# Performance work log

Hardware: AMD Instinct MI355X
Metric: run time of the kernel (lower is better)

Reference implementation:

```python
import jax, jax.numpy as jnp
import numpy as np

B, S, D = 2, 2048, 1024
H = 16
HD = D // H

def setup_inputs() -> dict:
    key = jax.random.key(0)
    ks = jax.random.split(key, 6)
    sc = 0.02
    return {
        'x': jax.random.normal(ks[0], (B, S, D), jnp.float32),
        'Wq': jax.random.normal(ks[1], (D, D), jnp.float32) * sc,
        'Wk': jax.random.normal(ks[2], (D, D), jnp.float32) * sc,
        'Wv': jax.random.normal(ks[3], (D, D), jnp.float32) * sc,
        'Wo': jax.random.normal(ks[4], (D, D), jnp.float32) * sc,
        'bo': jnp.zeros((D,), jnp.float32),
    }

def reference(x, Wq, Wk, Wv, Wo, bo):
    b, s, d_in = x.shape
    # torch Linear: y = x @ W.T
    q = jnp.einsum('bsd,ed->bse', x, Wq)
    k = jnp.einsum('bsd,ed->bse', x, Wk)
    v = jnp.einsum('bsd,ed->bse', x, Wv)
    # [b, h, s, hd]
    q = q.reshape(b, s, H, HD).transpose(0, 2, 1, 3)
    k = k.reshape(b, s, H, HD).transpose(0, 2, 1, 3)
    v = v.reshape(b, s, H, HD).transpose(0, 2, 1, 3)
    # NOTE: original divides by sqrt(d_out), not sqrt(head_dim)
    scores = jnp.einsum('bhqd,bhkd->bhqk', q, k) / jnp.sqrt(jnp.float32(D))
    causal = jnp.tril(jnp.ones((s, s), dtype=bool))  # True = keep
    scores = jnp.where(causal[None, None], scores, -jnp.inf)
    attn = jax.nn.softmax(scores, axis=-1)
    ctx = jnp.einsum('bhqk,bhkd->bhqd', attn, v)
    ctx = ctx.transpose(0, 2, 1, 3).reshape(b, s, D)
    return jnp.einsum('bsd,ed->bse', ctx, Wo) + bo
```

## Files before the change

kernel.cpp:

```cpp
#include <hip/hip_runtime.h>
#include <hip/hip_bf16.h>
#include <stdint.h>

typedef unsigned short u16;
typedef __attribute__((ext_vector_type(8))) short short8;
typedef __attribute__((ext_vector_type(4))) float f32x4;
typedef __attribute__((ext_vector_type(16))) float f32x16;
typedef __attribute__((ext_vector_type(4))) u16 u16x4;

#define NB 2
#define NS 2048
#define ND 1024
#define NH 16
#define NM 4096

#define QSCALE 0.045084220f

#if __has_builtin(__builtin_amdgcn_exp2f)
#define EXP2(x) __builtin_amdgcn_exp2f(x)
#else
__device__ __forceinline__ float __exp2_asm(float x){
  float r;
  asm("v_exp_f32 %0, %1" : "=v"(r) : "v"(x));
  return r;
}
#define EXP2(x) __exp2_asm(x)
#endif
#if __has_builtin(__builtin_amdgcn_rcpf)
#define RCP(x) __builtin_amdgcn_rcpf(x)
#else
#define RCP(x) (1.0f / (x))
#endif

__device__ __forceinline__ u16 f2bf(float f){
  union { float f; unsigned u; } v; v.f = f;
  unsigned r = v.u + 0x7fff + ((v.u >> 16) & 1);
  return (u16)(r >> 16);
}

__device__ __forceinline__ unsigned cvtpk(float lo, float hi){
  unsigned r;
  asm("v_cvt_pk_bf16_f32 %0, %1, %2" : "=v"(r) : "v"(lo), "v"(hi));
  return r;
}

__device__ __forceinline__ void pl32swap(unsigned &e, unsigned &o){
  asm("v_permlane32_swap_b32 %0, %1" : "+v"(e), "+v"(o));
}

__device__ __forceinline__ void gload_lds16(const u16* g, u16* l){
  __builtin_amdgcn_global_load_lds(
      (const __attribute__((address_space(1))) unsigned int*)g,
      (__attribute__((address_space(3))) unsigned int*)l, 16, 0, 0);
}

__device__ __forceinline__ f32x16 mfma32(short8 a, short8 b, f32x16 c){
  return __builtin_amdgcn_mfma_f32_32x32x16_bf16(a, b, c, 0, 0, 0);
}

__global__ void cvt_kernel(const float* __restrict__ src, u16* __restrict__ dst, int n){
  int i = (blockIdx.x * blockDim.x + threadIdx.x) * 4;
  if (i < n){
    float4 v = *(const float4*)(src + i);
    u16x4 o = { f2bf(v.x), f2bf(v.y), f2bf(v.z), f2bf(v.w) };
    *(u16x4*)(dst + i) = o;
  }
}

__global__ void cvt4_kernel(const float* __restrict__ a, const float* __restrict__ b,
                            const float* __restrict__ c, const float* __restrict__ d,
                            u16* __restrict__ oa, u16* __restrict__ ob,
                            u16* __restrict__ oc, u16* __restrict__ od){
  const float* s; u16* o;
  switch (blockIdx.y){
    case 0: s = a; o = oa; break;
    case 1: s = b; o = ob; break;
    case 2: s = c; o = oc; break;
    default: s = d; o = od; break;
  }
  int i = (blockIdx.x * blockDim.x + threadIdx.x) * 4;
  float4 v = *(const float4*)(s + i);
  u16x4 pk = { f2bf(v.x), f2bf(v.y), f2bf(v.z), f2bf(v.w) };
  *(u16x4*)(o + i) = pk;
}

__device__ __forceinline__ void gemm_core(
    const u16* __restrict__ A, const u16* __restrict__ W,
    int m0, int n0, u16* lsA, u16* lsB, f32x4 acc[4][4])
{
  const int tid = threadIdx.x;
  const int l   = tid & 63;
  const int wr  = (tid >> 7) & 1;
  const int wc  = (tid >> 6) & 1;
  const int lr  = l & 15;
  const int lkb = (l >> 4) << 4;
  const int sr  = tid >> 3;
  const int scb = (tid & 7) << 4;

  for (int kt = 0; kt < 16; ++kt){
    const int k0 = kt << 6;
    #pragma unroll
    for (int i = 0; i < 4; ++i){
      int r   = (i << 5) + sr;
      int cbs = scb ^ ((r & 7) << 4);
      gload_lds16(&A[(size_t)(m0 + r) * ND + k0 + (cbs >> 1)], &lsA[r * 64 + (scb >> 1)]);
      gload_lds16(&W[(size_t)(n0 + r) * ND + k0 + (cbs >> 1)], &lsB[r * 64 + (scb >> 1)]);
    }
    __syncthreads();

    short8 af[4][2], bf[4][2];
    #pragma unroll
    for (int m16 = 0; m16 < 4; ++m16){
      int r  = (wr << 6) + (m16 << 4) + lr;
      int rx = (r & 7) << 4;
      #pragma unroll
      for (int ks = 0; ks < 2; ++ks){
        int off = r * 128 + (((ks << 6) + lkb) ^ rx);
        af[m16][ks] = *(const short8*)((const char*)lsA + off);
      }
    }
    #pragma unroll
    for (int n16 = 0; n16 < 4; ++n16){
      int r  = (wc << 6) + (n16 << 4) + lr;
      int rx = (r & 7) << 4;
      #pragma unroll
      for (int ks = 0; ks < 2; ++ks){
        int off = r * 128 + (((ks << 6) + lkb) ^ rx);
        bf[n16][ks] = *(const short8*)((const char*)lsB + off);
      }
    }
    #pragma unroll
    for (int m16 = 0; m16 < 4; ++m16)
      #pragma unroll
      for (int n16 = 0; n16 < 4; ++n16){
        acc[m16][n16] = __builtin_amdgcn_mfma_f32_16x16x32_bf16(af[m16][0], bf[n16][0], acc[m16][n16], 0, 0, 0);
        acc[m16][n16] = __builtin_amdgcn_mfma_f32_16x16x32_bf16(af[m16][1], bf[n16][1], acc[m16][n16], 0, 0, 0);
      }
    __syncthreads();
  }
}

__global__ __launch_bounds__(256) void gemm_qkv(
    const u16* __restrict__ xb,
    const u16* __restrict__ Wqb, const u16* __restrict__ Wkb, const u16* __restrict__ Wvb,
    u16* __restrict__ Qo, u16* __restrict__ Ko, u16* __restrict__ Vt)
{
  __shared__ u16 lsA[128*64];
  __shared__ u16 lsB[128*64];
  const int z = blockIdx.z;
  const u16* W = (z == 0) ? Wqb : (z == 1) ? Wkb : Wvb;
  const int m0 = blockIdx.x << 7, n0 = blockIdx.y << 7;
  f32x4 acc[4][4] = {};
  gemm_core(xb, W, m0, n0, lsA, lsB, acc);

  const int l  = threadIdx.x & 63;
  const int wr = (threadIdx.x >> 7) & 1, wc = (threadIdx.x >> 6) & 1;
  const int rb = m0 + (wr << 6) + ((l >> 4) << 2);
  const int cb = n0 + (wc << 6) + (l & 15);

  if (z < 2){
    const float sc = (z == 0) ? QSCALE : 1.0f;
    u16* C = (z == 0) ? Qo : Ko;
    #pragma unroll
    for (int m16 = 0; m16 < 4; ++m16)
      #pragma unroll
      for (int n16 = 0; n16 < 4; ++n16)
        #pragma unroll
        for (int r = 0; r < 4; ++r)
          C[(size_t)(rb + (m16 << 4) + r) * ND + cb + (n16 << 4)] = f2bf(acc[m16][n16][r] * sc);
  } else {
    #pragma unroll
    for (int m16 = 0; m16 < 4; ++m16){
      int srow = rb + (m16 << 4);
      int bi = srow >> 11, s = srow & 2047;
      #pragma unroll
      for (int n16 = 0; n16 < 4; ++n16){
        int col = cb + (n16 << 4);
        u16x4 pk = { f2bf(acc[m16][n16][0]), f2bf(acc[m16][n16][1]),
                     f2bf(acc[m16][n16][2]), f2bf(acc[m16][n16][3]) };
        *(u16x4*)&Vt[((size_t)(bi * 16 + (col >> 6)) * 64 + (col & 63)) * 2048 + s] = pk;
      }
    }
  }
}

__global__ __launch_bounds__(256) void gemm_out(
    const u16* __restrict__ ctxb, const u16* __restrict__ Wob,
    const float* __restrict__ bo, float* __restrict__ out)
{
  __shared__ u16 lsA[128*64];
  __shared__ u16 lsB[128*64];
  const int m0 = blockIdx.x << 7, n0 = blockIdx.y << 7;
  f32x4 acc[4][4] = {};
  gemm_core(ctxb, Wob, m0, n0, lsA, lsB, acc);

  const int l  = threadIdx.x & 63;
  const int wr = (threadIdx.x >> 7) & 1, wc = (threadIdx.x >> 6) & 1;
  const int rb = m0 + (wr << 6) + ((l >> 4) << 2);
  const int cb = n0 + (wc << 6) + (l & 15);
  #pragma unroll
  for (int m16 = 0; m16 < 4; ++m16)
    #pragma unroll
    for (int n16 = 0; n16 < 4; ++n16)
      #pragma unroll
      for (int r = 0; r < 4; ++r){
        int col = cb + (n16 << 4);
        out[(size_t)(rb + (m16 << 4) + r) * ND + col] = acc[m16][n16][r] + bo[col];
      }
}

__device__ __forceinline__ void stage_tile(const u16* src, int srcStride, u16* lds, int tid){
  const int rl = tid >> 3;
  const int ch = tid & 7;
  const int cs = ch ^ (rl & 7);
  gload_lds16(&src[(size_t)rl * srcStride + cs * 8],        &lds[rl * 64 + ch * 8]);
  gload_lds16(&src[(size_t)(rl + 32) * srcStride + cs * 8], &lds[(rl + 32) * 64 + ch * 8]);
}

__device__ __forceinline__ void qk_tile(const u16* lsKt, const short8 qf[4],
                                        int q5, int hi, f32x16 &s0, f32x16 &s1){
  const char* Kc = (const char*)lsKt;
  const int swz = q5 & 7;
  f32x16 a = {}, b = {};
  __builtin_amdgcn_s_setprio(1);
  #pragma unroll
  for (int ks = 0; ks < 4; ++ks){
    int c0 = ((2 * ks + hi) ^ swz) << 4;
    short8 k0 = *(const short8*)(Kc + q5 * 128 + c0);
    short8 k1 = *(const short8*)(Kc + (q5 + 32) * 128 + c0);
    a = mfma32(k0, qf[ks], a);
    b = mfma32(k1, qf[ks], b);
  }
  __builtin_amdgcn_s_setprio(0);
  s0 = a; s1 = b;
}

__device__ __forceinline__ void sm_pv(f32x16 s0, f32x16 s1, const u16* lsVt,
                                      int t, int qb, int qgl, int q5, int hi,
                                      float &m_r, float &l_r, f32x16 &accA, f32x16 &accB){
  if (t * 64 + 63 > qb){
    #pragma unroll
    for (int r = 0; r < 16; ++r){
      int kl = t * 64 + (r & 3) + 8 * (r >> 2) + 4 * hi;
      if (kl > qgl)      s0[r] = -3e38f;
      if (kl + 32 > qgl) s1[r] = -3e38f;
    }
  }
  float mx[16];
  #pragma unroll
  for (int r = 0; r < 16; ++r) mx[r] = fmaxf(s0[r], s1[r]);
  #pragma unroll
  for (int stp = 8; stp > 0; stp >>= 1)
    #pragma unroll
    for (int r = 0; r < stp; ++r) mx[r] = fmaxf(mx[r], mx[r + stp]);
  float pm = fmaxf(mx[0], __shfl_xor(mx[0], 32));

  if (__any(pm > m_r + 8.f)){
    float mn = fmaxf(m_r, pm);
    float e  = EXP2(m_r - mn);
    m_r = mn; l_r *= e;
    #pragma unroll
    for (int r = 0; r < 16; ++r){ accA[r] *= e; accB[r] *= e; }
  }

  #pragma unroll
  for (int r = 0; r < 16; ++r){
    s0[r] = EXP2(s0[r] - m_r);
    s1[r] = EXP2(s1[r] - m_r);
  }
  float sm[16];
  #pragma unroll
  for (int r = 0; r < 16; ++r) sm[r] = s0[r] + s1[r];
  #pragma unroll
  for (int stp = 8; stp > 0; stp >>= 1)
    #pragma unroll
    for (int r = 0; r < stp; ++r) sm[r] += sm[r + stp];
  l_r += sm[0] + __shfl_xor(sm[0], 32);

  unsigned pw[2][4][2];
  #pragma unroll
  for (int g = 0; g < 4; ++g){
    pw[0][g][0] = cvtpk(s0[4*g],     s0[4*g + 1]);
    pw[0][g][1] = cvtpk(s0[4*g + 2], s0[4*g + 3]);
    pw[1][g][0] = cvtpk(s1[4*g],     s1[4*g + 1]);
    pw[1][g][1] = cvtpk(s1[4*g + 2], s1[4*g + 3]);
  }
  #pragma unroll
  for (int m = 0; m < 2; ++m)
    #pragma unroll
    for (int kp = 0; kp < 2; ++kp)
      #pragma unroll
      for (int i = 0; i < 2; ++i)
        pl32swap(pw[m][2*kp][i], pw[m][2*kp + 1][i]);

  const char* Vc = (const char*)lsVt;
  const int swz = q5 & 7;
  __builtin_amdgcn_s_setprio(1);
  #pragma unroll
  for (int ks = 0; ks < 4; ++ks){
    const int m = ks >> 1, kp = ks & 1;
    union { unsigned u[4]; short8 s8; } pa;
    pa.u[0] = pw[m][2*kp][0];
    pa.u[1] = pw[m][2*kp][1];
    pa.u[2] = pw[m][2*kp + 1][0];
    pa.u[3] = pw[m][2*kp + 1][1];
    int c0 = ((2 * ks + hi) ^ swz) << 4;
    short8 v0 = *(const short8*)(Vc + q5 * 128 + c0);
    short8 v1 = *(const short8*)(Vc + (q5 + 32) * 128 + c0);
    accA = mfma32(pa.s8, v0, accA);
    accB = mfma32(pa.s8, v1, accB);
  }
  __builtin_amdgcn_s_setprio(0);
}

__global__ __launch_bounds__(256, 2) void attn_kernel(
    const u16* __restrict__ Q, const u16* __restrict__ K,
    const u16* __restrict__ Vt, u16* __restrict__ ctx)
{
  __shared__ __align__(16) u16 lsK[3][64*64];
  __shared__ __align__(16) u16 lsV[3][64*64];

  const int bid = blockIdx.x;
  const int xcd = bid & 7;
  const int j   = bid >> 3;
  const int bh  = xcd + 8 * (j >> 4);
  const int st  = 15 - (j & 15);
  const int b = bh >> 4, h = bh & 15;
  const int tid = threadIdx.x;
  const int l = tid & 63, w = tid >> 6;
  const int q5 = l & 31, hi = l >> 5;
  const int qb   = st * 128 + w * 32;
  const int qgl  = qb + q5;
  const int nc   = (qb + 31) >> 6;
  const int tb   = 2 * st + 1;

  const u16* Kb0 = &K[(size_t)(b * NS) * ND + h * 64];
  const u16* Vb0 = &Vt[(size_t)bh * 64 * NS];

  short8 qf[4];
  {
    const u16* Qrow = &Q[(size_t)(b * NS + qgl) * ND + h * 64 + hi * 8];
    #pragma unroll
    for (int ks = 0; ks < 4; ++ks)
      qf[ks] = *(const short8*)&Qrow[ks * 16];
  }

  float m_r = -3e38f, l_r = 0.f;
  f32x16 accA = {}, accB = {};
  f32x16 sA0, sA1, sB0, sB1;

  stage_tile(Kb0, ND, lsK[0], tid);
  stage_tile(Vb0, NS, lsV[0], tid);
  stage_tile(&Kb0[(size_t)64 * ND], ND, lsK[1], tid);
  stage_tile(&Vb0[64],              NS, lsV[1], tid);
  __syncthreads();
  qk_tile(lsK[0], qf, q5, hi, sA0, sA1);

  #pragma unroll 1
  for (int t = 0; t <= tb; t += 2){
    {
      const int rs = (t + 2) % 3, rn = (t + 1) % 3, rc = t % 3;
      if (t + 2 <= tb){
        stage_tile(&Kb0[(size_t)(t + 2) * 64 * ND], ND, lsK[rs], tid);
        stage_tile(&Vb0[(t + 2) * 64],              NS, lsV[rs], tid);
      }
      if (t + 1 <= nc) qk_tile(lsK[rn], qf, q5, hi, sB0, sB1);
      if (t <= nc)     sm_pv(sA0, sA1, lsV[rc], t, qb, qgl, q5, hi, m_r, l_r, accA, accB);
      __syncthreads();
    }
    {
      const int t1 = t + 1;
      const int rs = (t1 + 2) % 3, rn = (t1 + 1) % 3, rc = t1 % 3;
      if (t1 + 2 <= tb){
        stage_tile(&Kb0[(size_t)(t1 + 2) * 64 * ND], ND, lsK[rs], tid);
        stage_tile(&Vb0[(t1 + 2) * 64],              NS, lsV[rs], tid);
      }
      if (t1 + 1 <= nc) qk_tile(lsK[rn], qf, q5, hi, sA0, sA1);
      if (t1 <= nc)     sm_pv(sB0, sB1, lsV[rc], t1, qb, qgl, q5, hi, m_r, l_r, accA, accB);
      __syncthreads();
    }
  }

  float inv = RCP(l_r);
  #pragma unroll
  for (int r = 0; r < 16; ++r){
    int qrow = (r & 3) + 8 * (r >> 2) + 4 * hi;
    float iv = __shfl(inv, (l & 32) | qrow, 64);
    u16* crow = &ctx[(size_t)(b * NS + qb + qrow) * ND + h * 64 + q5];
    crow[0]  = f2bf(accA[r] * iv);
    crow[32] = f2bf(accB[r] * iv);
  }
}

extern "C" void kernel_launch(void* const* d_in, const int* in_sizes, int n_in,
                              void* d_out, int out_size, void* d_ws, size_t ws_size,
                              hipStream_t stream)
{
  const float* x  = (const float*)d_in[0];
  const float* Wq = (const float*)d_in[1];
  const float* Wk = (const float*)d_in[2];
  const float* Wv = (const float*)d_in[3];
  const float* Wo = (const float*)d_in[4];
  const float* bo = (const float*)d_in[5];
  float* out = (float*)d_out;
  char* ws = (char*)d_ws;

  u16* xb  = (u16*)(ws);
  u16* Wqb = (u16*)(ws + (8u  << 20));
  u16* Wkb = (u16*)(ws + (10u << 20));
  u16* Wvb = (u16*)(ws + (12u << 20));
  u16* Wob = (u16*)(ws + (14u << 20));
  u16* Qb  = (u16*)(ws + (16u << 20));
  u16* Kb  = (u16*)(ws + (24u << 20));
  u16* Vtb = (u16*)(ws + (32u << 20));
  u16* Cb  = (u16*)(ws + (40u << 20));

  cvt_kernel<<<4096, 256, 0, stream>>>(x, xb, NM * ND);
  cvt4_kernel<<<dim3(1024, 4), 256, 0, stream>>>(Wq, Wk, Wv, Wo, Wqb, Wkb, Wvb, Wob);

  gemm_qkv<<<dim3(32, 8, 3), 256, 0, stream>>>(xb, Wqb, Wkb, Wvb, Qb, Kb, Vtb);
  attn_kernel<<<512, 256, 0, stream>>>(Qb, Kb, Vtb, Cb);
  gemm_out<<<dim3(32, 8), 256, 0, stream>>>(Cb, Wob, bo, out);
}
```

Before: 133.8 us.

## Deepen K/V LDS ring to four stages with partial vmcnt waits

Grows the K/V shared-memory ring buffer from three to four tiles and prefetches three tiles ahead instead of two. The full __syncthreads is replaced by an explicit s_waitcnt vmcnt(4) plus s_barrier, so each barrier waits only for the older tile's loads while the newest prefetch stays in flight. This is meant to hide global load latency better. In exchange LDS per block rises from 48 KB to 64 KB, which may limit occupancy, and the hand-set vmcnt count depends on stage_tile issuing exactly four loads per thread.

```diff
diff --git a/kernel.cpp b/kernel.cpp
--- a/kernel.cpp
+++ b/kernel.cpp
@@ -313,12 +313,29 @@
   __builtin_amdgcn_s_setprio(0);
 }
 
+#define SUBITER(T, SC0, SC1, SN0, SN1)                                            \
+  {                                                                               \
+    const int t_ = (T);                                                           \
+    if (t_ + 3 <= tb){                                                            \
+      stage_tile(&Kb0[(size_t)(t_ + 3) * 64 * ND], ND, lsK[(t_ + 3) & 3], tid);   \
+      stage_tile(&Vb0[(t_ + 3) * 64],              NS, lsV[(t_ + 3) & 3], tid);   \
+    }                                                                             \
+    if (t_ + 1 <= nc) qk_tile(lsK[(t_ + 1) & 3], qf, q5, hi, SN0, SN1);           \
+    if (t_ <= nc)     sm_pv(SC0, SC1, lsV[t_ & 3], t_, qb, qgl, q5, hi,           \
+                            m_r, l_r, accA, accB);                                \
+    if (t_ + 3 <= tb) asm volatile("s_waitcnt vmcnt(4)" ::: "memory");            \
+    else              asm volatile("s_waitcnt vmcnt(0)" ::: "memory");            \
+    __builtin_amdgcn_sched_barrier(0);                                            \
+    __builtin_amdgcn_s_barrier();                                                 \
+    __builtin_amdgcn_sched_barrier(0);                                            \
+  }
+
 __global__ __launch_bounds__(256, 2) void attn_kernel(
     const u16* __restrict__ Q, const u16* __restrict__ K,
     const u16* __restrict__ Vt, u16* __restrict__ ctx)
 {
-  __shared__ __align__(16) u16 lsK[3][64*64];
-  __shared__ __align__(16) u16 lsV[3][64*64];
+  __shared__ __align__(16) u16 lsK[4][64*64];
+  __shared__ __align__(16) u16 lsV[4][64*64];
 
   const int bid = blockIdx.x;
   const int xcd = bid & 7;
@@ -353,32 +370,22 @@
   stage_tile(Vb0, NS, lsV[0], tid);
   stage_tile(&Kb0[(size_t)64 * ND], ND, lsK[1], tid);
   stage_tile(&Vb0[64],              NS, lsV[1], tid);
-  __syncthreads();
+  if (2 <= tb){
+    stage_tile(&Kb0[(size_t)128 * ND], ND, lsK[2], tid);
+    stage_tile(&Vb0[128],              NS, lsV[2], tid);
+    asm volatile("s_waitcnt vmcnt(4)" ::: "memory");
+  } else {
+    asm volatile("s_waitcnt vmcnt(0)" ::: "memory");
+  }
+  __builtin_amdgcn_sched_barrier(0);
+  __builtin_amdgcn_s_barrier();
+  __builtin_amdgcn_sched_barrier(0);
   qk_tile(lsK[0], qf, q5, hi, sA0, sA1);
 
   #pragma unroll 1
   for (int t = 0; t <= tb; t += 2){
-    {
-      const int rs = (t + 2) % 3, rn = (t + 1) % 3, rc = t % 3;
-      if (t + 2 <= tb){
-        stage_tile(&Kb0[(size_t)(t + 2) * 64 * ND], ND, lsK[rs], tid);
-        stage_tile(&Vb0[(t + 2) * 64],              NS, lsV[rs], tid);
-      }
-      if (t + 1 <= nc) qk_tile(lsK[rn], qf, q5, hi, sB0, sB1);
-      if (t <= nc)     sm_pv(sA0, sA1, lsV[rc], t, qb, qgl, q5, hi, m_r, l_r, accA, accB);
-      __syncthreads();
-    }
-    {
-      const int t1 = t + 1;
-      const int rs = (t1 + 2) % 3, rn = (t1 + 1) % 3, rc = t1 % 3;
-      if (t1 + 2 <= tb){
-        stage_tile(&Kb0[(size_t)(t1 + 2) * 64 * ND], ND, lsK[rs], tid);
-        stage_tile(&Vb0[(t1 + 2) * 64],              NS, lsV[rs], tid);
-      }
-      if (t1 + 1 <= nc) qk_tile(lsK[rn], qf, q5, hi, sA0, sA1);
-      if (t1 <= nc)     sm_pv(sB0, sB1, lsV[rc], t1, qb, qgl, q5, hi, m_r, l_r, accA, accB);
-      __syncthreads();
-    }
+    SUBITER(t,     sA0, sA1, sB0, sB1);
+    SUBITER(t + 1, sB0, sB1, sA0, sA1);
   }
 
   float inv = RCP(l_r);
```

Measured after the change: 133.4 us. No clear change (-0.2%).

## Split KV range across warp groups in attention and merge partial softmax states

Applied to the files above, without the earlier changes.

Restructures the attention kernel so each block handles 64 query rows, with two warp groups splitting the causal key range and merging their partial max/sum/accumulators through shared memory at the end. V fragments are loaded directly from global memory into registers instead of being staged through LDS, which cuts LDS to double-buffered K tiles. The grid doubles to 1024 blocks with launch bounds of 4 blocks per CU to raise occupancy. The cost is uncached direct V loads, a merge step, and the removal of the previous QK/PV software pipeline.

```diff
diff --git a/kernel.cpp b/kernel.cpp
--- a/kernel.cpp
+++ b/kernel.cpp
@@ -235,8 +235,8 @@
   s0 = a; s1 = b;
 }
 
-__device__ __forceinline__ void sm_pv(f32x16 s0, f32x16 s1, const u16* lsVt,
-                                      int t, int qb, int qgl, int q5, int hi,
+__device__ __forceinline__ void sm_pv(f32x16 s0, f32x16 s1, const short8 vf[4][2],
+                                      int t, int qb, int qgl, int hi,
                                       float &m_r, float &l_r, f32x16 &accA, f32x16 &accB){
   if (t * 64 + 63 > qb){
     #pragma unroll
@@ -293,8 +293,6 @@
       for (int i = 0; i < 2; ++i)
         pl32swap(pw[m][2*kp][i], pw[m][2*kp + 1][i]);
 
-  const char* Vc = (const char*)lsVt;
-  const int swz = q5 & 7;
   __builtin_amdgcn_s_setprio(1);
   #pragma unroll
   for (int ks = 0; ks < 4; ++ks){
@@ -304,35 +302,36 @@
     pa.u[1] = pw[m][2*kp][1];
     pa.u[2] = pw[m][2*kp + 1][0];
     pa.u[3] = pw[m][2*kp + 1][1];
-    int c0 = ((2 * ks + hi) ^ swz) << 4;
-    short8 v0 = *(const short8*)(Vc + q5 * 128 + c0);
-    short8 v1 = *(const short8*)(Vc + (q5 + 32) * 128 + c0);
-    accA = mfma32(pa.s8, v0, accA);
-    accB = mfma32(pa.s8, v1, accB);
+    accA = mfma32(pa.s8, vf[ks][0], accA);
+    accB = mfma32(pa.s8, vf[ks][1], accB);
   }
   __builtin_amdgcn_s_setprio(0);
 }
 
-__global__ __launch_bounds__(256, 2) void attn_kernel(
+__global__ __launch_bounds__(256, 4) void attn_kernel(
     const u16* __restrict__ Q, const u16* __restrict__ K,
     const u16* __restrict__ Vt, u16* __restrict__ ctx)
 {
-  __shared__ __align__(16) u16 lsK[3][64*64];
-  __shared__ __align__(16) u16 lsV[3][64*64];
+  __shared__ __align__(16) u16 lsK[2][2][64*64];
 
   const int bid = blockIdx.x;
   const int xcd = bid & 7;
   const int j   = bid >> 3;
-  const int bh  = xcd + 8 * (j >> 4);
-  const int st  = 15 - (j & 15);
+  const int cu  = j & 31;
+  const int wrap= j >> 5;
+  const int st  = (wrap & 1) ? cu : (31 - cu);
+  const int bh  = xcd + 8 * wrap;
   const int b = bh >> 4, h = bh & 15;
   const int tid = threadIdx.x;
   const int l = tid & 63, w = tid >> 6;
   const int q5 = l & 31, hi = l >> 5;
-  const int qb   = st * 128 + w * 32;
-  const int qgl  = qb + q5;
-  const int nc   = (qb + 31) >> 6;
-  const int tb   = 2 * st + 1;
+  const int qsub = w & 1, grp = w >> 1;
+  const int qb  = st * 64 + qsub * 32;
+  const int qgl = qb + q5;
+  const int n0  = (st + 2) >> 1;
+  const int n1  = st + 1 - n0;
+  const int tOff = grp ? n0 : 0;
+  const int nMy  = grp ? n1 : n0;
 
   const u16* Kb0 = &K[(size_t)(b * NS) * ND + h * 64];
   const u16* Vb0 = &Vt[(size_t)bh * 64 * NS];
@@ -347,48 +346,67 @@
 
   float m_r = -3e38f, l_r = 0.f;
   f32x16 accA = {}, accB = {};
-  f32x16 sA0, sA1, sB0, sB1;
-
-  stage_tile(Kb0, ND, lsK[0], tid);
-  stage_tile(Vb0, NS, lsV[0], tid);
-  stage_tile(&Kb0[(size_t)64 * ND], ND, lsK[1], tid);
-  stage_tile(&Vb0[64],              NS, lsV[1], tid);
+
+  stage_tile(Kb0, ND, lsK[0][0], tid);
+  if (n1 > 0) stage_tile(&Kb0[(size_t)n0 * 64 * ND], ND, lsK[1][0], tid);
   __syncthreads();
-  qk_tile(lsK[0], qf, q5, hi, sA0, sA1);
 
   #pragma unroll 1
-  for (int t = 0; t <= tb; t += 2){
-    {
-      const int rs = (t + 2) % 3, rn = (t + 1) % 3, rc = t % 3;
-      if (t + 2 <= tb){
-        stage_tile(&Kb0[(size_t)(t + 2) * 64 * ND], ND, lsK[rs], tid);
-        stage_tile(&Vb0[(t + 2) * 64],              NS, lsV[rs], tid);
-      }
-      if (t + 1 <= nc) qk_tile(lsK[rn], qf, q5, hi, sB0, sB1);
-      if (t <= nc)     sm_pv(sA0, sA1, lsV[rc], t, qb, qgl, q5, hi, m_r, l_r, accA, accB);
-      __syncthreads();
-    }
-    {
-      const int t1 = t + 1;
-      const int rs = (t1 + 2) % 3, rn = (t1 + 1) % 3, rc = t1 % 3;
-      if (t1 + 2 <= tb){
-        stage_tile(&Kb0[(size_t)(t1 + 2) * 64 * ND], ND, lsK[rs], tid);
-        stage_tile(&Vb0[(t1 + 2) * 64],              NS, lsV[rs], tid);
-      }
-      if (t1 + 1 <= nc) qk_tile(lsK[rn], qf, q5, hi, sA0, sA1);
-      if (t1 <= nc)     sm_pv(sB0, sB1, lsV[rc], t1, qb, qgl, q5, hi, m_r, l_r, accA, accB);
-      __syncthreads();
-    }
-  }
-
-  float inv = RCP(l_r);
-  #pragma unroll
-  for (int r = 0; r < 16; ++r){
-    int qrow = (r & 3) + 8 * (r >> 2) + 4 * hi;
-    float iv = __shfl(inv, (l & 32) | qrow, 64);
-    u16* crow = &ctx[(size_t)(b * NS + qb + qrow) * ND + h * 64 + q5];
-    crow[0]  = f2bf(accA[r] * iv);
-    crow[32] = f2bf(accB[r] * iv);
+  for (int i = 0; i < n0; ++i){
+    const int rc = i & 1;
+    const int myT = tOff + i;
+    const bool act = (i < nMy);
+
+    short8 vf[4][2];
+    if (act){
+      const u16* vb = Vb0 + (size_t)myT * 64;
+      #pragma unroll
+      for (int ks = 0; ks < 4; ++ks){
+        vf[ks][0] = *(const short8*)&vb[(size_t)q5 * NS + (2 * ks + hi) * 8];
+        vf[ks][1] = *(const short8*)&vb[(size_t)(q5 + 32) * NS + (2 * ks + hi) * 8];
+      }
+    }
+    if (i + 1 < n0)
+      stage_tile(&Kb0[(size_t)(i + 1) * 64 * ND], ND, lsK[0][rc ^ 1], tid);
+    if (n0 + i + 1 <= st)
+      stage_tile(&Kb0[(size_t)(n0 + i + 1) * 64 * ND], ND, lsK[1][rc ^ 1], tid);
+
+    if (act){
+      f32x16 s0, s1;
+      qk_tile(lsK[grp][rc], qf, q5, hi, s0, s1);
+      sm_pv(s0, s1, vf, myT, qb, qgl, hi, m_r, l_r, accA, accB);
+    }
+    __syncthreads();
+  }
+
+  float* mb = (float*)&lsK[0][0][0];
+  if (grp == 1){
+    int base = ((w - 2) * 64 + l) * 34;
+    mb[base] = m_r; mb[base + 1] = l_r;
+    #pragma unroll
+    for (int r = 0; r < 16; ++r){ mb[base + 2 + r] = accA[r]; mb[base + 18 + r] = accB[r]; }
+  }
+  __syncthreads();
+  if (grp == 0){
+    int base = (w * 64 + l) * 34;
+    float m1 = mb[base], l1 = mb[base + 1];
+    float m  = fmaxf(m_r, m1);
+    float e0 = EXP2(m_r - m), e1 = EXP2(m1 - m);
+    float lm = l_r * e0 + l1 * e1;
+    float inv = RCP(lm);
+    #pragma unroll
+    for (int r = 0; r < 16; ++r){
+      accA[r] = accA[r] * e0 + mb[base + 2 + r]  * e1;
+      accB[r] = accB[r] * e0 + mb[base + 18 + r] * e1;
+    }
+    #pragma unroll
+    for (int r = 0; r < 16; ++r){
+      int qrow = (r & 3) + 8 * (r >> 2) + 4 * hi;
+      float iv = __shfl(inv, (l & 32) | qrow, 64);
+      u16* crow = &ctx[(size_t)(b * NS + qb + qrow) * ND + h * 64 + q5];
+      crow[0]  = f2bf(accA[r] * iv);
+      crow[32] = f2bf(accB[r] * iv);
+    }
   }
 }
 
@@ -419,6 +437,6 @@
   cvt4_kernel<<<dim3(1024, 4), 256, 0, stream>>>(Wq, Wk, Wv, Wo, Wqb, Wkb, Wvb, Wob);
 
   gemm_qkv<<<dim3(32, 8, 3), 256, 0, stream>>>(xb, Wqb, Wkb, Wvb, Qb, Kb, Vtb);
-  attn_kernel<<<512, 256, 0, stream>>>(Qb, Kb, Vtb, Cb);
+  attn_kernel<<<1024, 256, 0, stream>>>(Qb, Kb, Vtb, Cb);
   gemm_out<<<dim3(32, 8), 256, 0, stream>>>(Cb, Wob, bo, out);
 }
```

Result: slower. 152.2 us (+13.8%).

## Shrink attention blocks to 64 queries with double buffering and merge conversion kernels

Applied to the files above, without the earlier changes.

Each attention block now holds 2 waves (128 threads) covering 64 queries instead of 4 waves covering 128, and the launch doubles to 1024 blocks. The triple-buffered, software-pipelined QK/PV loop becomes a simpler double-buffered loop that stages the next K/V tile while computing the current one. The two fp32-to-bf16 conversion kernels are also merged into one launch. The aim is finer causal load balancing and more resident blocks, but it gives up the overlap of the next tile's QK with the current softmax/PV and doubles K/V reloads per head.

```diff
diff --git a/kernel.cpp b/kernel.cpp
--- a/kernel.cpp
+++ b/kernel.cpp
@@ -58,30 +58,24 @@
   return __builtin_amdgcn_mfma_f32_32x32x16_bf16(a, b, c, 0, 0, 0);
 }
 
-__global__ void cvt_kernel(const float* __restrict__ src, u16* __restrict__ dst, int n){
-  int i = (blockIdx.x * blockDim.x + threadIdx.x) * 4;
-  if (i < n){
-    float4 v = *(const float4*)(src + i);
-    u16x4 o = { f2bf(v.x), f2bf(v.y), f2bf(v.z), f2bf(v.w) };
-    *(u16x4*)(dst + i) = o;
-  }
-}
-
-__global__ void cvt4_kernel(const float* __restrict__ a, const float* __restrict__ b,
-                            const float* __restrict__ c, const float* __restrict__ d,
-                            u16* __restrict__ oa, u16* __restrict__ ob,
-                            u16* __restrict__ oc, u16* __restrict__ od){
-  const float* s; u16* o;
-  switch (blockIdx.y){
-    case 0: s = a; o = oa; break;
-    case 1: s = b; o = ob; break;
-    case 2: s = c; o = oc; break;
-    default: s = d; o = od; break;
-  }
-  int i = (blockIdx.x * blockDim.x + threadIdx.x) * 4;
+__global__ void cvt_all(const float* __restrict__ x,
+                        const float* __restrict__ wq, const float* __restrict__ wk,
+                        const float* __restrict__ wv, const float* __restrict__ wo,
+                        u16* __restrict__ xb, u16* __restrict__ wqb, u16* __restrict__ wkb,
+                        u16* __restrict__ wvb, u16* __restrict__ wob){
+  int ib = blockIdx.x;
+  const float* s; u16* d; int off;
+  if (ib < 4096){ s = x; d = xb; off = ib; }
+  else {
+    int t = ib - 4096, sel = t >> 10;
+    off = t & 1023;
+    s = (sel == 0) ? wq : (sel == 1) ? wk : (sel == 2) ? wv : wo;
+    d = (sel == 0) ? wqb : (sel == 1) ? wkb : (sel == 2) ? wvb : wob;
+  }
+  int i = (off * 256 + threadIdx.x) * 4;
   float4 v = *(const float4*)(s + i);
   u16x4 pk = { f2bf(v.x), f2bf(v.y), f2bf(v.z), f2bf(v.w) };
-  *(u16x4*)(o + i) = pk;
+  *(u16x4*)(d + i) = pk;
 }
 
 __device__ __forceinline__ void gemm_core(
@@ -209,12 +203,15 @@
       }
 }
 
-__device__ __forceinline__ void stage_tile(const u16* src, int srcStride, u16* lds, int tid){
+__device__ __forceinline__ void stage128(const u16* src, int srcStride, u16* lds, int tid){
   const int rl = tid >> 3;
   const int ch = tid & 7;
-  const int cs = ch ^ (rl & 7);
-  gload_lds16(&src[(size_t)rl * srcStride + cs * 8],        &lds[rl * 64 + ch * 8]);
-  gload_lds16(&src[(size_t)(rl + 32) * srcStride + cs * 8], &lds[(rl + 32) * 64 + ch * 8]);
+  #pragma unroll
+  for (int k = 0; k < 4; ++k){
+    int rr = rl + 16 * k;
+    int cs = ch ^ (rr & 7);
+    gload_lds16(&src[(size_t)rr * srcStride + cs * 8], &lds[rr * 64 + ch * 8]);
+  }
 }
 
 __device__ __forceinline__ void qk_tile(const u16* lsKt, const short8 qf[4],
@@ -313,26 +310,26 @@
   __builtin_amdgcn_s_setprio(0);
 }
 
-__global__ __launch_bounds__(256, 2) void attn_kernel(
+__global__ __launch_bounds__(128) void attn_kernel(
     const u16* __restrict__ Q, const u16* __restrict__ K,
     const u16* __restrict__ Vt, u16* __restrict__ ctx)
 {
-  __shared__ __align__(16) u16 lsK[3][64*64];
-  __shared__ __align__(16) u16 lsV[3][64*64];
+  __shared__ __align__(16) u16 lsK[2][64*64];
+  __shared__ __align__(16) u16 lsV[2][64*64];
 
   const int bid = blockIdx.x;
   const int xcd = bid & 7;
   const int j   = bid >> 3;
-  const int bh  = xcd + 8 * (j >> 4);
-  const int st  = 15 - (j & 15);
+  const int strm = j >> 5;
+  const int st   = 31 - (j & 31);
+  const int bh   = xcd + 8 * strm;
   const int b = bh >> 4, h = bh & 15;
   const int tid = threadIdx.x;
   const int l = tid & 63, w = tid >> 6;
   const int q5 = l & 31, hi = l >> 5;
-  const int qb   = st * 128 + w * 32;
-  const int qgl  = qb + q5;
-  const int nc   = (qb + 31) >> 6;
-  const int tb   = 2 * st + 1;
+  const int qb  = st * 64 + w * 32;
+  const int qgl = qb + q5;
+  const int tb  = st;
 
   const u16* Kb0 = &K[(size_t)(b * NS) * ND + h * 64];
   const u16* Vb0 = &Vt[(size_t)bh * 64 * NS];
@@ -347,38 +344,22 @@
 
   float m_r = -3e38f, l_r = 0.f;
   f32x16 accA = {}, accB = {};
-  f32x16 sA0, sA1, sB0, sB1;
-
-  stage_tile(Kb0, ND, lsK[0], tid);
-  stage_tile(Vb0, NS, lsV[0], tid);
-  stage_tile(&Kb0[(size_t)64 * ND], ND, lsK[1], tid);
-  stage_tile(&Vb0[64],              NS, lsV[1], tid);
+
+  stage128(Kb0, ND, lsK[0], tid);
+  stage128(Vb0, NS, lsV[0], tid);
   __syncthreads();
-  qk_tile(lsK[0], qf, q5, hi, sA0, sA1);
 
   #pragma unroll 1
-  for (int t = 0; t <= tb; t += 2){
-    {
-      const int rs = (t + 2) % 3, rn = (t + 1) % 3, rc = t % 3;
-      if (t + 2 <= tb){
-        stage_tile(&Kb0[(size_t)(t + 2) * 64 * ND], ND, lsK[rs], tid);
-        stage_tile(&Vb0[(t + 2) * 64],              NS, lsV[rs], tid);
-      }
-      if (t + 1 <= nc) qk_tile(lsK[rn], qf, q5, hi, sB0, sB1);
-      if (t <= nc)     sm_pv(sA0, sA1, lsV[rc], t, qb, qgl, q5, hi, m_r, l_r, accA, accB);
-      __syncthreads();
-    }
-    {
-      const int t1 = t + 1;
-      const int rs = (t1 + 2) % 3, rn = (t1 + 1) % 3, rc = t1 % 3;
-      if (t1 + 2 <= tb){
-        stage_tile(&Kb0[(size_t)(t1 + 2) * 64 * ND], ND, lsK[rs], tid);
-        stage_tile(&Vb0[(t1 + 2) * 64],              NS, lsV[rs], tid);
-      }
-      if (t1 + 1 <= nc) qk_tile(lsK[rn], qf, q5, hi, sA0, sA1);
-      if (t1 <= nc)     sm_pv(sB0, sB1, lsV[rc], t1, qb, qgl, q5, hi, m_r, l_r, accA, accB);
-      __syncthreads();
-    }
+  for (int t = 0; t <= tb; ++t){
+    const int rc = t & 1;
+    if (t < tb){
+      stage128(&Kb0[(size_t)(t + 1) * 64 * ND], ND, lsK[rc ^ 1], tid);
+      stage128(&Vb0[(t + 1) * 64],              NS, lsV[rc ^ 1], tid);
+    }
+    f32x16 s0, s1;
+    qk_tile(lsK[rc], qf, q5, hi, s0, s1);
+    sm_pv(s0, s1, lsV[rc], t, qb, qgl, q5, hi, m_r, l_r, accA, accB);
+    __syncthreads();
   }
 
   float inv = RCP(l_r);
@@ -415,10 +396,9 @@
   u16* Vtb = (u16*)(ws + (32u << 20));
   u16* Cb  = (u16*)(ws + (40u << 20));
 
-  cvt_kernel<<<4096, 256, 0, stream>>>(x, xb, NM * ND);
-  cvt4_kernel<<<dim3(1024, 4), 256, 0, stream>>>(Wq, Wk, Wv, Wo, Wqb, Wkb, Wvb, Wob);
+  cvt_all<<<8192, 256, 0, stream>>>(x, Wq, Wk, Wv, Wo, xb, Wqb, Wkb, Wvb, Wob);
 
   gemm_qkv<<<dim3(32, 8, 3), 256, 0, stream>>>(xb, Wqb, Wkb, Wvb, Qb, Kb, Vtb);
-  attn_kernel<<<512, 256, 0, stream>>>(Qb, Kb, Vtb, Cb);
+  attn_kernel<<<1024, 128, 0, stream>>>(Qb, Kb, Vtb, Cb);
   gemm_out<<<dim3(32, 8), 256, 0, stream>>>(Cb, Wob, bo, out);
 }
```

New measurement: 139.7 us. 1.04x slower.
